# Kernel optimization log

Measured on AMD Instinct MI355X. Metric: run time of the kernel, lower is better.

Reference implementation:

```python
import jax, jax.numpy as jnp
import numpy as np

WS = 8          # window size
NH = 8          # num heads
DIM = 256
HD = DIM // NH  # head dim = 32
SCALE = HD ** -0.5
EPS = 1e-5


def _rel_pos_index(ws):
    # deterministic int index buffer, same math as the torch __init__
    coords = jnp.stack(jnp.meshgrid(jnp.arange(ws), jnp.arange(ws), indexing='ij'))  # [2,ws,ws]
    cf = coords.reshape(2, -1)                     # [2, N]
    rel = cf[:, :, None] - cf[:, None, :]          # [2, N, N]
    return (rel[0] + ws - 1) * (2 * ws - 1) + (rel[1] + ws - 1)  # [N, N]


def _ln(h, g, b):
    m = jnp.mean(h, axis=-1, keepdims=True)
    v = jnp.mean((h - m) ** 2, axis=-1, keepdims=True)
    return (h - m) / jnp.sqrt(v + EPS) * g + b


def setup_inputs() -> dict:
    key = jax.random.key(0)
    ks = jax.random.split(key, 16)
    B_, N, D = 4096, WS * WS, DIM
    s = 0.02
    return {
        'x':      jax.random.normal(ks[0], (B_, N, D), jnp.float32),
        # enhanced qkv: Linear(D,2D) -> LN -> GELU -> Linear(2D,3D)
        'w_qkv1': jax.random.normal(ks[1], (D, 2 * D), jnp.float32) * s,
        'b_qkv1': jnp.zeros((2 * D,), jnp.float32),
        'g_qkv':  jnp.ones((2 * D,), jnp.float32),
        'be_qkv': jnp.zeros((2 * D,), jnp.float32),
        'w_qkv2': jax.random.normal(ks[2], (2 * D, 3 * D), jnp.float32) * s,
        'b_qkv2': jnp.zeros((3 * D,), jnp.float32),
        # relative position bias table [(2*WS-1)^2, NH]
        'rpb':    jax.random.normal(ks[3], ((2 * WS - 1) ** 2, NH), jnp.float32) * s,
        # enhanced proj: Linear(D,2D) -> LN -> GELU -> Linear(2D,D)
        'w_p1':   jax.random.normal(ks[4], (D, 2 * D), jnp.float32) * s,
        'b_p1':   jnp.zeros((2 * D,), jnp.float32),
        'g_p':    jnp.ones((2 * D,), jnp.float32),
        'be_p':   jnp.zeros((2 * D,), jnp.float32),
        'w_p2':   jax.random.normal(ks[5], (2 * D, D), jnp.float32) * s,
        'b_p2':   jnp.zeros((D,), jnp.float32),
    }


def reference(x, w_qkv1, b_qkv1, g_qkv, be_qkv, w_qkv2, b_qkv2, rpb,
              w_p1, b_p1, g_p, be_p, w_p2, b_p2):
    B_, N, C = x.shape
    # enhanced QKV chain: Linear -> LayerNorm -> GELU -> Linear
    h = jax.nn.gelu(_ln(x @ w_qkv1 + b_qkv1, g_qkv, be_qkv), approximate=False)
    qkv = h @ w_qkv2 + b_qkv2                              # [B_, N, 3C]
    qkv = qkv.reshape(B_, N, 3, NH, HD).transpose(2, 0, 3, 1, 4)  # [3, B_, H, N, hd]
    q, k, v = qkv[0], qkv[1], qkv[2]
    attn = jnp.einsum('bhnd,bhmd->bhnm', q * SCALE, k)     # [B_, H, N, N]
    idx = _rel_pos_index(WS)                                # [N, N] int
    bias = rpb[idx.reshape(-1)].reshape(N, N, NH).transpose(2, 0, 1)  # [H, N, N]
    attn = jax.nn.softmax(attn + bias[None], axis=-1)
    out = jnp.einsum('bhnm,bhmd->bhnd', attn, v)           # [B_, H, N, hd]
    out = out.transpose(0, 2, 1, 3).reshape(B_, N, C)
    # enhanced proj chain: Linear -> LayerNorm -> GELU -> Linear
    h = jax.nn.gelu(_ln(out @ w_p1 + b_p1, g_p, be_p), approximate=False)
    return h @ w_p2 + b_p2
```

## Files before the change

kernel.cpp:

```cpp
#include <hip/hip_runtime.h>


typedef __bf16 bf16_t;
typedef __bf16 bf16x8 __attribute__((ext_vector_type(8)));
typedef __bf16 bf16x4 __attribute__((ext_vector_type(4)));
typedef float f32x4 __attribute__((ext_vector_type(4)));

__device__ __forceinline__ f32x4 mfma16(bf16x8 a, bf16x8 b, f32x4 acc) {
  return __builtin_amdgcn_mfma_f32_16x16x32_bf16(a, b, acc, 0, 0, 0);
}

#define SWZ(row, byteoff) ((byteoff) ^ (((row) & 7) << 4))

__device__ __forceinline__ float gelu_f(float v) {
  float e = __expf(v * (1.59576912f + 0.07135482f * v * v));
  return v - v * __builtin_amdgcn_rcpf(1.0f + e);
}

__global__ void wtrans_kernel(const float* __restrict__ src, bf16_t* __restrict__ dst,
                              int kshift, int N, int total) {
  int i = blockIdx.x * 256 + threadIdx.x;
  if (i >= total) return;
  int K = 1 << kshift;
  int k = i & (K - 1);
  int n = i >> kshift;
  dst[i] = (bf16_t)src[(size_t)k * N + n];
}

__device__ __forceinline__ void gemmT_ln_gelu(
    const char* bsrc, const bf16_t* __restrict__ wt,
    const float* __restrict__ bias, const float* __restrict__ gamma,
    const float* __restrict__ beta,
    char* dst, int flb, float2* part, int wave, int g, int c)
{
  f32x4 acc[4][4] = {};
#pragma unroll
  for (int kt = 0; kt < 8; ++kt) {
    bf16x8 a[4], b[4];
#pragma unroll
    for (int mt = 0; mt < 4; ++mt)
      a[mt] = *(const bf16x8*)(wt + (size_t)(wave * 64 + mt * 16 + c) * 256 + kt * 32 + g * 8);
#pragma unroll
    for (int nt = 0; nt < 4; ++nt) {
      int T = nt * 16 + c;
      b[nt] = *(const bf16x8*)(bsrc + SWZ(T, T * 512 + kt * 64 + g * 16));
    }
#pragma unroll
    for (int mt = 0; mt < 4; ++mt)
#pragma unroll
      for (int nt = 0; nt < 4; ++nt)
        acc[mt][nt] = mfma16(a[mt], b[nt], acc[mt][nt]);
  }
  float s[4] = {0.f, 0.f, 0.f, 0.f}, ss[4] = {0.f, 0.f, 0.f, 0.f};
#pragma unroll
  for (int mt = 0; mt < 4; ++mt) {
    float4 b4 = *(const float4*)(bias + wave * 64 + mt * 16 + g * 4);
#pragma unroll
    for (int nt = 0; nt < 4; ++nt)
#pragma unroll
      for (int r = 0; r < 4; ++r) {
        float v = acc[mt][nt][r] + ((const float*)&b4)[r];
        acc[mt][nt][r] = v;
        s[nt] += v;
        ss[nt] += v * v;
      }
  }
#pragma unroll
  for (int nt = 0; nt < 4; ++nt) {
    float sv = s[nt], ssv = ss[nt];
    sv += __shfl_xor(sv, 16, 64); ssv += __shfl_xor(ssv, 16, 64);
    sv += __shfl_xor(sv, 32, 64); ssv += __shfl_xor(ssv, 32, 64);
    if (g == 0) part[wave * 64 + nt * 16 + c] = make_float2(sv, ssv);
  }
  __syncthreads();
#pragma unroll
  for (int nt = 0; nt < 4; ++nt) {
    float sv = 0.f, ssv = 0.f;
#pragma unroll
    for (int w = 0; w < 8; ++w) {
      float2 p2 = part[w * 64 + nt * 16 + c];
      sv += p2.x; ssv += p2.y;
    }
    float m = sv * (1.f / 512.f);
    float rstd = rsqrtf(ssv * (1.f / 512.f) - m * m + 1e-5f);
#pragma unroll
    for (int mt = 0; mt < 4; ++mt)
#pragma unroll
      for (int r = 0; r < 4; ++r)
        acc[mt][nt][r] = (acc[mt][nt][r] - m) * rstd;
  }
#pragma unroll
  for (int mt = 0; mt < 4; ++mt) {
    float4 g4 = *(const float4*)(gamma + wave * 64 + mt * 16 + g * 4);
    float4 be4 = *(const float4*)(beta + wave * 64 + mt * 16 + g * 4);
    int f0 = flb + mt * 16 + g * 4;
#pragma unroll
    for (int nt = 0; nt < 4; ++nt) {
      int T = nt * 16 + c;
      bf16x4 h4;
#pragma unroll
      for (int r = 0; r < 4; ++r) {
        float v = acc[mt][nt][r] * ((const float*)&g4)[r] + ((const float*)&be4)[r];
        h4[r] = (bf16_t)gelu_f(v);
      }
      *(bf16x4*)(dst + SWZ(T, T * 512 + f0 * 2)) = h4;
    }
  }
}

__device__ __forceinline__ void dump_h(const char* rA, const char* rB,
                                       bf16_t* __restrict__ hg, int win, int tid)
{
#pragma unroll
  for (int it = 0; it < 8; ++it) {
    int byte = it * 8192 + tid * 16;
    int T = byte >> 10, off = byte & 1023;
    const char* src = (off < 512) ? (rB + SWZ(T, T * 512 + off))
                                  : (rA + SWZ(T, T * 512 + off - 512));
    *(bf16x8*)((char*)hg + (size_t)(win * 64 + T) * 1024 + off) = *(const bf16x8*)src;
  }
}

__global__ __launch_bounds__(512, 2) void g1_kernel(
    const float* __restrict__ x,
    const bf16_t* __restrict__ w1t, const float* __restrict__ b1,
    const float* __restrict__ g1, const float* __restrict__ be1,
    bf16_t* __restrict__ hg)
{
  __shared__ __align__(16) char sm[69632];
  char* rA = sm;
  char* rB = sm + 32768;
  float2* part = (float2*)(sm + 65536);
  const int tid = threadIdx.x;
  const int wave = tid >> 6, lane = tid & 63;
  const int g = lane >> 4, c = lane & 15;
  const int win = blockIdx.x;

  const float* xw = x + (size_t)win * 16384;
#pragma unroll
  for (int it = 0; it < 8; ++it) {
    int e = it * 2048 + tid * 4;
    float4 v = *(const float4*)(xw + e);
    int row = e >> 8, col = e & 255;
    bf16x4 t4;
    t4[0] = (bf16_t)v.x; t4[1] = (bf16_t)v.y; t4[2] = (bf16_t)v.z; t4[3] = (bf16_t)v.w;
    *(bf16x4*)(rA + SWZ(row, row * 512 + col * 2)) = t4;
  }
  __syncthreads();
  gemmT_ln_gelu(rA, w1t, b1, g1, be1, (wave < 4) ? rB : rA, (wave & 3) * 64,
                part, wave, g, c);
  __syncthreads();
  dump_h(rA, rB, hg, win, tid);
}

__global__ __launch_bounds__(512, 2) void g3_kernel(
    const bf16_t* __restrict__ ao,
    const bf16_t* __restrict__ wp1t, const float* __restrict__ bp1,
    const float* __restrict__ gp, const float* __restrict__ bep,
    bf16_t* __restrict__ h2g)
{
  __shared__ __align__(16) char sm[69632];
  char* rA = sm;
  char* rB = sm + 32768;
  float2* part = (float2*)(sm + 65536);
  const int tid = threadIdx.x;
  const int wave = tid >> 6, lane = tid & 63;
  const int g = lane >> 4, c = lane & 15;
  const int win = blockIdx.x;

  const bf16_t* aow = ao + (size_t)win * 16384;
#pragma unroll
  for (int it = 0; it < 4; ++it) {
    int e = it * 4096 + tid * 8;
    bf16x8 v = *(const bf16x8*)(aow + e);
    int row = e >> 8, col = e & 255;
    *(bf16x8*)(rA + SWZ(row, row * 512 + col * 2)) = v;
  }
  __syncthreads();
  gemmT_ln_gelu(rA, wp1t, bp1, gp, bep, (wave < 4) ? rB : rA, (wave & 3) * 64,
                part, wave, g, c);
  __syncthreads();
  dump_h(rA, rB, h2g, win, tid);
}

__global__ __launch_bounds__(512, 2) void qkv_attn_kernel(
    const bf16_t* __restrict__ hg,
    const bf16_t* __restrict__ w2t, const float* __restrict__ b2,
    const float* __restrict__ rpb,
    bf16_t* __restrict__ ao)
{
  __shared__ __align__(16) char sm[81920];
  char* hs = sm;
  char* ded = sm + 65536;
  const int tid = threadIdx.x;
  const int wave = tid >> 6, lane = tid & 63;
  const int g = lane >> 4, c = lane & 15;
  const int win = blockIdx.x;
  const int head = wave;

  const char* hw = (const char*)(hg + (size_t)win * 32768);
#pragma unroll
  for (int it = 0; it < 8; ++it) {
    int byte = it * 8192 + tid * 16;
    int T = byte >> 10, off = byte & 1023;
    *(bf16x8*)(hs + SWZ(T, T * 1024 + off)) = *(const bf16x8*)(hw + byte);
  }
  __syncthreads();

  bf16x4 vreg[2][4], qreg[2][4], kreg[2][4];

  {
    f32x4 acc[2][4] = {};
#pragma unroll
    for (int kt = 0; kt < 16; ++kt) {
      bf16x8 a[2], b[4];
#pragma unroll
      for (int mt = 0; mt < 2; ++mt)
        a[mt] = *(const bf16x8*)(w2t + (size_t)(512 + head * 32 + mt * 16 + c) * 512 + kt * 32 + g * 8);
#pragma unroll
      for (int nt = 0; nt < 4; ++nt) {
        int T = nt * 16 + c;
        b[nt] = *(const bf16x8*)(hs + SWZ(T, T * 1024 + kt * 64 + g * 16));
      }
#pragma unroll
      for (int mt = 0; mt < 2; ++mt)
#pragma unroll
        for (int nt = 0; nt < 4; ++nt)
          acc[mt][nt] = mfma16(a[mt], b[nt], acc[mt][nt]);
    }
    if (head < 4) {
      char* vs = ded + head * 4096;
#pragma unroll
      for (int mt = 0; mt < 2; ++mt) {
        float4 b4 = *(const float4*)(b2 + 512 + head * 32 + mt * 16 + g * 4);
#pragma unroll
        for (int nt = 0; nt < 4; ++nt) {
          int T = nt * 16 + c;
#pragma unroll
          for (int r = 0; r < 4; ++r) {
            int d = mt * 16 + g * 4 + r;
            *(bf16_t*)(vs + SWZ(d, d * 128 + T * 2)) =
                (bf16_t)(acc[mt][nt][r] + ((const float*)&b4)[r]);
          }
        }
      }
    } else {
#pragma unroll
      for (int mt = 0; mt < 2; ++mt) {
        float4 b4 = *(const float4*)(b2 + 512 + head * 32 + mt * 16 + g * 4);
#pragma unroll
        for (int nt = 0; nt < 4; ++nt) {
          bf16x4 o4;
#pragma unroll
          for (int r = 0; r < 4; ++r)
            o4[r] = (bf16_t)(acc[mt][nt][r] + ((const float*)&b4)[r]);
          vreg[mt][nt] = o4;
        }
      }
    }
  }
  {
    f32x4 acc[2][4] = {};
#pragma unroll
    for (int kt = 0; kt < 16; ++kt) {
      bf16x8 a[2], b[4];
#pragma unroll
      for (int mt = 0; mt < 2; ++mt)
        a[mt] = *(const bf16x8*)(w2t + (size_t)(head * 32 + mt * 16 + c) * 512 + kt * 32 + g * 8);
#pragma unroll
      for (int nt = 0; nt < 4; ++nt) {
        int T = nt * 16 + c;
        b[nt] = *(const bf16x8*)(hs + SWZ(T, T * 1024 + kt * 64 + g * 16));
      }
#pragma unroll
      for (int mt = 0; mt < 2; ++mt)
#pragma unroll
        for (int nt = 0; nt < 4; ++nt)
          acc[mt][nt] = mfma16(a[mt], b[nt], acc[mt][nt]);
    }
#pragma unroll
    for (int mt = 0; mt < 2; ++mt) {
      float4 b4 = *(const float4*)(b2 + head * 32 + mt * 16 + g * 4);
#pragma unroll
      for (int nt = 0; nt < 4; ++nt) {
        bf16x4 o4;
#pragma unroll
        for (int r = 0; r < 4; ++r)
          o4[r] = (bf16_t)((acc[mt][nt][r] + ((const float*)&b4)[r]) * 0.17677669529663687f);
        qreg[mt][nt] = o4;
      }
    }
  }
  {
    f32x4 acc[2][4] = {};
#pragma unroll
    for (int kt = 0; kt < 16; ++kt) {
      bf16x8 a[2], b[4];
#pragma unroll
      for (int mt = 0; mt < 2; ++mt)
        a[mt] = *(const bf16x8*)(w2t + (size_t)(256 + head * 32 + mt * 16 + c) * 512 + kt * 32 + g * 8);
#pragma unroll
      for (int nt = 0; nt < 4; ++nt) {
        int T = nt * 16 + c;
        b[nt] = *(const bf16x8*)(hs + SWZ(T, T * 1024 + kt * 64 + g * 16));
      }
#pragma unroll
      for (int mt = 0; mt < 2; ++mt)
#pragma unroll
        for (int nt = 0; nt < 4; ++nt)
          acc[mt][nt] = mfma16(a[mt], b[nt], acc[mt][nt]);
    }
#pragma unroll
    for (int mt = 0; mt < 2; ++mt) {
      float4 b4 = *(const float4*)(b2 + 256 + head * 32 + mt * 16 + g * 4);
#pragma unroll
      for (int nt = 0; nt < 4; ++nt) {
        bf16x4 o4;
#pragma unroll
        for (int r = 0; r < 4; ++r)
          o4[r] = (bf16_t)(acc[mt][nt][r] + ((const float*)&b4)[r]);
        kreg[mt][nt] = o4;
      }
    }
  }
  __syncthreads();

  {
    char* qb = sm + (head & 3) * 8192 + (head >> 2) * 32768;
#pragma unroll
    for (int mt = 0; mt < 2; ++mt)
#pragma unroll
      for (int nt = 0; nt < 4; ++nt) {
        int T = nt * 16 + c, d0 = mt * 16 + g * 4;
        *(bf16x4*)(qb + SWZ(T, T * 64 + d0 * 2)) = qreg[mt][nt];
        *(bf16x4*)(qb + 4096 + SWZ(T, T * 64 + d0 * 2)) = kreg[mt][nt];
      }
  }
  __syncthreads();

  const int rowbase = (wave >> 2) * 32;
#pragma unroll
  for (int s = 0; s < 2; ++s) {
    const int hd = s * 4 + (wave & 3);
    char* qb = sm + (wave & 3) * 8192 + s * 32768;
    char* vslot = ded + (wave & 3) * 4096;

    bf16x8 aq[2], bk[4];
#pragma unroll
    for (int mt = 0; mt < 2; ++mt) {
      int t = rowbase + mt * 16 + c;
      aq[mt] = *(const bf16x8*)(qb + SWZ(t, t * 64 + g * 16));
    }
#pragma unroll
    for (int nt = 0; nt < 4; ++nt) {
      int t = nt * 16 + c;
      bk[nt] = *(const bf16x8*)(qb + 4096 + SWZ(t, t * 64 + g * 16));
    }
    float p[2][4][4];
#pragma unroll
    for (int mt = 0; mt < 2; ++mt)
#pragma unroll
      for (int nt = 0; nt < 4; ++nt) {
        f32x4 z = {0.f, 0.f, 0.f, 0.f};
        f32x4 s4 = mfma16(aq[mt], bk[nt], z);
#pragma unroll
        for (int r = 0; r < 4; ++r) {
          int i = rowbase + mt * 16 + g * 4 + r, j = nt * 16 + c;
          int idx = ((i >> 3) - (j >> 3) + 7) * 15 + ((i & 7) - (j & 7) + 7);
          p[mt][nt][r] = s4[r] + rpb[idx * 8 + hd];
        }
      }
#pragma unroll
    for (int mt = 0; mt < 2; ++mt)
#pragma unroll
      for (int r = 0; r < 4; ++r) {
        float mx = fmaxf(fmaxf(p[mt][0][r], p[mt][1][r]), fmaxf(p[mt][2][r], p[mt][3][r]));
#pragma unroll
        for (int m = 1; m < 16; m <<= 1) mx = fmaxf(mx, __shfl_xor(mx, m, 64));
        float sum = 0.f;
#pragma unroll
        for (int nt = 0; nt < 4; ++nt) {
          float e = __expf(p[mt][nt][r] - mx);
          p[mt][nt][r] = e; sum += e;
        }
#pragma unroll
        for (int m = 1; m < 16; m <<= 1) sum += __shfl_xor(sum, m, 64);
        float rinv = 1.f / sum;
#pragma unroll
        for (int nt = 0; nt < 4; ++nt) p[mt][nt][r] *= rinv;
      }
    __syncthreads();
#pragma unroll
    for (int mt = 0; mt < 2; ++mt)
#pragma unroll
      for (int nt = 0; nt < 4; ++nt)
#pragma unroll
        for (int r = 0; r < 4; ++r) {
          int i = rowbase + mt * 16 + g * 4 + r, j = nt * 16 + c;
          *(bf16_t*)(qb + SWZ(i, i * 128 + j * 2)) = (bf16_t)p[mt][nt][r];
        }
    asm volatile("s_waitcnt lgkmcnt(0)" ::: "memory");
    f32x4 oacc[2][2] = {};
#pragma unroll
    for (int kp = 0; kp < 2; ++kp) {
      bf16x8 ap[2], bv[2];
#pragma unroll
      for (int mt = 0; mt < 2; ++mt) {
        int t = rowbase + mt * 16 + c;
        ap[mt] = *(const bf16x8*)(qb + SWZ(t, t * 128 + kp * 64 + g * 16));
      }
#pragma unroll
      for (int nt = 0; nt < 2; ++nt) {
        int d = nt * 16 + c;
        bv[nt] = *(const bf16x8*)(vslot + SWZ(d, d * 128 + kp * 64 + g * 16));
      }
#pragma unroll
      for (int mt = 0; mt < 2; ++mt)
#pragma unroll
        for (int nt = 0; nt < 2; ++nt)
          oacc[mt][nt] = mfma16(ap[mt], bv[nt], oacc[mt][nt]);
    }
#pragma unroll
    for (int mt = 0; mt < 2; ++mt)
#pragma unroll
      for (int nt = 0; nt < 2; ++nt)
#pragma unroll
        for (int r = 0; r < 4; ++r) {
          int T = rowbase + mt * 16 + g * 4 + r;
          ao[(size_t)(win * 64 + T) * 256 + hd * 32 + nt * 16 + c] = (bf16_t)oacc[mt][nt][r];
        }
    __syncthreads();
    if (s == 0) {
      if (head >= 4) {
        char* vs = ded + (head & 3) * 4096;
#pragma unroll
        for (int mt = 0; mt < 2; ++mt)
#pragma unroll
          for (int nt = 0; nt < 4; ++nt) {
            int T = nt * 16 + c;
#pragma unroll
            for (int r = 0; r < 4; ++r) {
              int d = mt * 16 + g * 4 + r;
              *(bf16_t*)(vs + SWZ(d, d * 128 + T * 2)) = vreg[mt][nt][r];
            }
          }
      }
      __syncthreads();
    }
  }
}

__global__ __launch_bounds__(512, 2) void g4_kernel(
    const bf16_t* __restrict__ h2g, const bf16_t* __restrict__ wp2t,
    const float* __restrict__ bp2, float* __restrict__ out)
{
  __shared__ __align__(16) char hs[65536];
  const int tid = threadIdx.x;
  const int wave = tid >> 6, lane = tid & 63;
  const int g = lane >> 4, c = lane & 15;
  const int win = blockIdx.x;

  const char* hw = (const char*)(h2g + (size_t)win * 32768);
#pragma unroll
  for (int it = 0; it < 8; ++it) {
    int byte = it * 8192 + tid * 16;
    int T = byte >> 10, off = byte & 1023;
    *(bf16x8*)(hs + SWZ(T, T * 1024 + off)) = *(const bf16x8*)(hw + byte);
  }
  __syncthreads();

  f32x4 acc[2][4] = {};
#pragma unroll
  for (int kt = 0; kt < 16; ++kt) {
    bf16x8 a[2], b[4];
#pragma unroll
    for (int mt = 0; mt < 2; ++mt)
      a[mt] = *(const bf16x8*)(wp2t + (size_t)(wave * 32 + mt * 16 + c) * 512 + kt * 32 + g * 8);
#pragma unroll
    for (int nt = 0; nt < 4; ++nt) {
      int T = nt * 16 + c;
      b[nt] = *(const bf16x8*)(hs + SWZ(T, T * 1024 + kt * 64 + g * 16));
    }
#pragma unroll
    for (int mt = 0; mt < 2; ++mt)
#pragma unroll
      for (int nt = 0; nt < 4; ++nt)
        acc[mt][nt] = mfma16(a[mt], b[nt], acc[mt][nt]);
  }
  float* ow = out + (size_t)win * 16384;
#pragma unroll
  for (int mt = 0; mt < 2; ++mt) {
    float4 b4 = *(const float4*)(bp2 + wave * 32 + mt * 16 + g * 4);
#pragma unroll
    for (int nt = 0; nt < 4; ++nt) {
      int T = nt * 16 + c;
      f32x4 o4;
#pragma unroll
      for (int r = 0; r < 4; ++r) o4[r] = acc[mt][nt][r] + ((const float*)&b4)[r];
      *(f32x4*)(ow + T * 256 + wave * 32 + mt * 16 + g * 4) = o4;
    }
  }
}

extern "C" void kernel_launch(void* const* d_in, const int* in_sizes, int n_in,
                              void* d_out, int out_size, void* d_ws, size_t ws_size,
                              hipStream_t stream) {
  const float* x   = (const float*)d_in[0];
  const float* w1  = (const float*)d_in[1];
  const float* b1  = (const float*)d_in[2];
  const float* g1  = (const float*)d_in[3];
  const float* be1 = (const float*)d_in[4];
  const float* w2  = (const float*)d_in[5];
  const float* b2  = (const float*)d_in[6];
  const float* rpb = (const float*)d_in[7];
  const float* wp1 = (const float*)d_in[8];
  const float* bp1 = (const float*)d_in[9];
  const float* gp  = (const float*)d_in[10];
  const float* bep = (const float*)d_in[11];
  const float* wp2 = (const float*)d_in[12];
  const float* bp2 = (const float*)d_in[13];
  float* out = (float*)d_out;
  char* ws = (char*)d_ws;
  bf16_t* w1t  = (bf16_t*)(ws + 0);
  bf16_t* w2t  = (bf16_t*)(ws + 262144);
  bf16_t* wp1t = (bf16_t*)(ws + 1048576);
  bf16_t* wp2t = (bf16_t*)(ws + 1310720);
  bf16_t* hg   = (bf16_t*)(ws + 2097152);
  bf16_t* ao   = (bf16_t*)(ws + 270532608);

  wtrans_kernel<<<512, 256, 0, stream>>>(w1, w1t, 8, 512, 131072);
  wtrans_kernel<<<1536, 256, 0, stream>>>(w2, w2t, 9, 768, 393216);
  wtrans_kernel<<<512, 256, 0, stream>>>(wp1, wp1t, 8, 512, 131072);
  wtrans_kernel<<<512, 256, 0, stream>>>(wp2, wp2t, 9, 256, 131072);

  g1_kernel<<<4096, 512, 0, stream>>>(x, w1t, b1, g1, be1, hg);
  qkv_attn_kernel<<<4096, 512, 0, stream>>>(hg, w2t, b2, rpb, ao);
  g3_kernel<<<4096, 512, 0, stream>>>(ao, wp1t, bp1, gp, bep, hg);
  g4_kernel<<<4096, 512, 0, stream>>>(hg, wp2t, bp2, out);
}
```

Measured before the change: 1.335 ms.

## Fuse first LN-GELU GEMM into QKV-attention and fuse both projection GEMMs

```diff
diff --git a/kernel.cpp b/kernel.cpp
--- a/kernel.cpp
+++ b/kernel.cpp
@@ -27,6 +27,13 @@
   dst[i] = (bf16_t)src[(size_t)k * N + n];
 }
 
+__global__ void biastab_kernel(const float* __restrict__ rpb, float* __restrict__ bt) {
+  int e = blockIdx.x * 256 + threadIdx.x;
+  int hd = e >> 12, i = (e >> 6) & 63, j = e & 63;
+  int idx = ((i >> 3) - (j >> 3) + 7) * 15 + ((i & 7) - (j & 7) + 7);
+  bt[e] = rpb[idx * 8 + hd];
+}
+
 __device__ __forceinline__ void gemmT_ln_gelu(
     const char* bsrc, const bf16_t* __restrict__ wt,
     const float* __restrict__ bias, const float* __restrict__ gamma,
@@ -108,24 +115,295 @@
   }
 }
 
-__device__ __forceinline__ void dump_h(const char* rA, const char* rB,
-                                       bf16_t* __restrict__ hg, int win, int tid)
-{
-#pragma unroll
-  for (int it = 0; it < 8; ++it) {
-    int byte = it * 8192 + tid * 16;
-    int T = byte >> 10, off = byte & 1023;
-    const char* src = (off < 512) ? (rB + SWZ(T, T * 512 + off))
-                                  : (rA + SWZ(T, T * 512 + off - 512));
-    *(bf16x8*)((char*)hg + (size_t)(win * 64 + T) * 1024 + off) = *(const bf16x8*)src;
-  }
-}
-
-__global__ __launch_bounds__(512, 2) void g1_kernel(
+__global__ __launch_bounds__(512, 4) void g1qa_kernel(
     const float* __restrict__ x,
     const bf16_t* __restrict__ w1t, const float* __restrict__ b1,
-    const float* __restrict__ g1, const float* __restrict__ be1,
-    bf16_t* __restrict__ hg)
+    const float* __restrict__ gamma1, const float* __restrict__ beta1,
+    const bf16_t* __restrict__ w2t, const float* __restrict__ b2,
+    const float* __restrict__ bt,
+    bf16_t* __restrict__ ao)
+{
+  __shared__ __align__(16) char sm[81920];
+  char* rA = sm;
+  char* rB = sm + 32768;
+  char* ded = sm + 65536;
+  float2* part = (float2*)ded;
+  const int tid = threadIdx.x;
+  const int wave = tid >> 6, lane = tid & 63;
+  const int g = lane >> 4, c = lane & 15;
+  const int win = blockIdx.x;
+  const int head = wave;
+
+  const float* xw = x + (size_t)win * 16384;
+#pragma unroll
+  for (int it = 0; it < 8; ++it) {
+    int e = it * 2048 + tid * 4;
+    float4 v = *(const float4*)(xw + e);
+    int row = e >> 8, col = e & 255;
+    bf16x4 t4;
+    t4[0] = (bf16_t)v.x; t4[1] = (bf16_t)v.y; t4[2] = (bf16_t)v.z; t4[3] = (bf16_t)v.w;
+    *(bf16x4*)(rA + SWZ(row, row * 512 + col * 2)) = t4;
+  }
+  __syncthreads();
+  gemmT_ln_gelu(rA, w1t, b1, gamma1, beta1, (wave < 4) ? rB : rA, (wave & 3) * 64,
+                part, wave, g, c);
+  __syncthreads();
+
+  bf16x4 vreg[2][4], qreg[2][4], kreg[2][4];
+
+  {
+    f32x4 acc[2][4] = {};
+#pragma unroll
+    for (int kt = 0; kt < 16; ++kt) {
+      const char* hb = (kt < 8) ? rB : rA;
+      const int ko = (kt & 7) * 64 + g * 16;
+      bf16x8 a[2], b[4];
+#pragma unroll
+      for (int mt = 0; mt < 2; ++mt)
+        a[mt] = *(const bf16x8*)(w2t + (size_t)(512 + head * 32 + mt * 16 + c) * 512 + kt * 32 + g * 8);
+#pragma unroll
+      for (int nt = 0; nt < 4; ++nt) {
+        int T = nt * 16 + c;
+        b[nt] = *(const bf16x8*)(hb + SWZ(T, T * 512 + ko));
+      }
+#pragma unroll
+      for (int mt = 0; mt < 2; ++mt)
+#pragma unroll
+        for (int nt = 0; nt < 4; ++nt)
+          acc[mt][nt] = mfma16(a[mt], b[nt], acc[mt][nt]);
+    }
+    if (head < 4) {
+      char* vs = ded + head * 4096;
+#pragma unroll
+      for (int mt = 0; mt < 2; ++mt) {
+        float4 b4 = *(const float4*)(b2 + 512 + head * 32 + mt * 16 + g * 4);
+#pragma unroll
+        for (int nt = 0; nt < 4; ++nt) {
+          int T = nt * 16 + c;
+#pragma unroll
+          for (int r = 0; r < 4; ++r) {
+            int d = mt * 16 + g * 4 + r;
+            *(bf16_t*)(vs + SWZ(d, d * 128 + T * 2)) =
+                (bf16_t)(acc[mt][nt][r] + ((const float*)&b4)[r]);
+          }
+        }
+      }
+    } else {
+#pragma unroll
+      for (int mt = 0; mt < 2; ++mt) {
+        float4 b4 = *(const float4*)(b2 + 512 + head * 32 + mt * 16 + g * 4);
+#pragma unroll
+        for (int nt = 0; nt < 4; ++nt) {
+          bf16x4 o4;
+#pragma unroll
+          for (int r = 0; r < 4; ++r)
+            o4[r] = (bf16_t)(acc[mt][nt][r] + ((const float*)&b4)[r]);
+          vreg[mt][nt] = o4;
+        }
+      }
+    }
+  }
+  {
+    f32x4 acc[2][4] = {};
+#pragma unroll
+    for (int kt = 0; kt < 16; ++kt) {
+      const char* hb = (kt < 8) ? rB : rA;
+      const int ko = (kt & 7) * 64 + g * 16;
+      bf16x8 a[2], b[4];
+#pragma unroll
+      for (int mt = 0; mt < 2; ++mt)
+        a[mt] = *(const bf16x8*)(w2t + (size_t)(head * 32 + mt * 16 + c) * 512 + kt * 32 + g * 8);
+#pragma unroll
+      for (int nt = 0; nt < 4; ++nt) {
+        int T = nt * 16 + c;
+        b[nt] = *(const bf16x8*)(hb + SWZ(T, T * 512 + ko));
+      }
+#pragma unroll
+      for (int mt = 0; mt < 2; ++mt)
+#pragma unroll
+        for (int nt = 0; nt < 4; ++nt)
+          acc[mt][nt] = mfma16(a[mt], b[nt], acc[mt][nt]);
+    }
+#pragma unroll
+    for (int mt = 0; mt < 2; ++mt) {
+      float4 b4 = *(const float4*)(b2 + head * 32 + mt * 16 + g * 4);
+#pragma unroll
+      for (int nt = 0; nt < 4; ++nt) {
+        bf16x4 o4;
+#pragma unroll
+        for (int r = 0; r < 4; ++r)
+          o4[r] = (bf16_t)((acc[mt][nt][r] + ((const float*)&b4)[r]) * 0.17677669529663687f);
+        qreg[mt][nt] = o4;
+      }
+    }
+  }
+  {
+    f32x4 acc[2][4] = {};
+#pragma unroll
+    for (int kt = 0; kt < 16; ++kt) {
+      const char* hb = (kt < 8) ? rB : rA;
+      const int ko = (kt & 7) * 64 + g * 16;
+      bf16x8 a[2], b[4];
+#pragma unroll
+      for (int mt = 0; mt < 2; ++mt)
+        a[mt] = *(const bf16x8*)(w2t + (size_t)(256 + head * 32 + mt * 16 + c) * 512 + kt * 32 + g * 8);
+#pragma unroll
+      for (int nt = 0; nt < 4; ++nt) {
+        int T = nt * 16 + c;
+        b[nt] = *(const bf16x8*)(hb + SWZ(T, T * 512 + ko));
+      }
+#pragma unroll
+      for (int mt = 0; mt < 2; ++mt)
+#pragma unroll
+        for (int nt = 0; nt < 4; ++nt)
+          acc[mt][nt] = mfma16(a[mt], b[nt], acc[mt][nt]);
+    }
+#pragma unroll
+    for (int mt = 0; mt < 2; ++mt) {
+      float4 b4 = *(const float4*)(b2 + 256 + head * 32 + mt * 16 + g * 4);
+#pragma unroll
+      for (int nt = 0; nt < 4; ++nt) {
+        bf16x4 o4;
+#pragma unroll
+        for (int r = 0; r < 4; ++r)
+          o4[r] = (bf16_t)(acc[mt][nt][r] + ((const float*)&b4)[r]);
+        kreg[mt][nt] = o4;
+      }
+    }
+  }
+  __syncthreads();
+
+  {
+    char* qb = sm + (head & 3) * 8192 + (head >> 2) * 32768;
+#pragma unroll
+    for (int mt = 0; mt < 2; ++mt)
+#pragma unroll
+      for (int nt = 0; nt < 4; ++nt) {
+        int T = nt * 16 + c, d0 = mt * 16 + g * 4;
+        *(bf16x4*)(qb + SWZ(T, T * 64 + d0 * 2)) = qreg[mt][nt];
+        *(bf16x4*)(qb + 4096 + SWZ(T, T * 64 + d0 * 2)) = kreg[mt][nt];
+      }
+  }
+  __syncthreads();
+
+  const int rowbase = (wave >> 2) * 32;
+#pragma unroll
+  for (int s = 0; s < 2; ++s) {
+    const int hd = s * 4 + (wave & 3);
+    char* qb = sm + (wave & 3) * 8192 + s * 32768;
+    char* vslot = ded + (wave & 3) * 4096;
+    const float* btab = bt + hd * 4096;
+
+    bf16x8 aq[2], bk[4];
+#pragma unroll
+    for (int mt = 0; mt < 2; ++mt) {
+      int t = rowbase + mt * 16 + c;
+      aq[mt] = *(const bf16x8*)(qb + SWZ(t, t * 64 + g * 16));
+    }
+#pragma unroll
+    for (int nt = 0; nt < 4; ++nt) {
+      int t = nt * 16 + c;
+      bk[nt] = *(const bf16x8*)(qb + 4096 + SWZ(t, t * 64 + g * 16));
+    }
+    float p[2][4][4];
+#pragma unroll
+    for (int mt = 0; mt < 2; ++mt)
+#pragma unroll
+      for (int nt = 0; nt < 4; ++nt) {
+        f32x4 z = {0.f, 0.f, 0.f, 0.f};
+        f32x4 s4 = mfma16(aq[mt], bk[nt], z);
+#pragma unroll
+        for (int r = 0; r < 4; ++r) {
+          int i = rowbase + mt * 16 + g * 4 + r, j = nt * 16 + c;
+          p[mt][nt][r] = s4[r] + btab[i * 64 + j];
+        }
+      }
+#pragma unroll
+    for (int mt = 0; mt < 2; ++mt)
+#pragma unroll
+      for (int r = 0; r < 4; ++r) {
+        float mx = fmaxf(fmaxf(p[mt][0][r], p[mt][1][r]), fmaxf(p[mt][2][r], p[mt][3][r]));
+#pragma unroll
+        for (int m = 1; m < 16; m <<= 1) mx = fmaxf(mx, __shfl_xor(mx, m, 64));
+        float sum = 0.f;
+#pragma unroll
+        for (int nt = 0; nt < 4; ++nt) {
+          float e = __expf(p[mt][nt][r] - mx);
+          p[mt][nt][r] = e; sum += e;
+        }
+#pragma unroll
+        for (int m = 1; m < 16; m <<= 1) sum += __shfl_xor(sum, m, 64);
+        float rinv = 1.f / sum;
+#pragma unroll
+        for (int nt = 0; nt < 4; ++nt) p[mt][nt][r] *= rinv;
+      }
+    __syncthreads();
+#pragma unroll
+    for (int mt = 0; mt < 2; ++mt)
+#pragma unroll
+      for (int nt = 0; nt < 4; ++nt)
+#pragma unroll
+        for (int r = 0; r < 4; ++r) {
+          int i = rowbase + mt * 16 + g * 4 + r, j = nt * 16 + c;
+          *(bf16_t*)(qb + SWZ(i, i * 128 + j * 2)) = (bf16_t)p[mt][nt][r];
+        }
+    asm volatile("s_waitcnt lgkmcnt(0)" ::: "memory");
+    f32x4 oacc[2][2] = {};
+#pragma unroll
+    for (int kp = 0; kp < 2; ++kp) {
+      bf16x8 ap[2], bv[2];
+#pragma unroll
+      for (int mt = 0; mt < 2; ++mt) {
+        int t = rowbase + mt * 16 + c;
+        ap[mt] = *(const bf16x8*)(qb + SWZ(t, t * 128 + kp * 64 + g * 16));
+      }
+#pragma unroll
+      for (int nt = 0; nt < 2; ++nt) {
+        int d = nt * 16 + c;
+        bv[nt] = *(const bf16x8*)(vslot + SWZ(d, d * 128 + kp * 64 + g * 16));
+      }
+#pragma unroll
+      for (int mt = 0; mt < 2; ++mt)
+#pragma unroll
+        for (int nt = 0; nt < 2; ++nt)
+          oacc[mt][nt] = mfma16(ap[mt], bv[nt], oacc[mt][nt]);
+    }
+#pragma unroll
+    for (int mt = 0; mt < 2; ++mt)
+#pragma unroll
+      for (int nt = 0; nt < 2; ++nt)
+#pragma unroll
+        for (int r = 0; r < 4; ++r) {
+          int T = rowbase + mt * 16 + g * 4 + r;
+          ao[(size_t)(win * 64 + T) * 256 + hd * 32 + nt * 16 + c] = (bf16_t)oacc[mt][nt][r];
+        }
+    __syncthreads();
+    if (s == 0) {
+      if (head >= 4) {
+        char* vs = ded + (head & 3) * 4096;
+#pragma unroll
+        for (int mt = 0; mt < 2; ++mt)
+#pragma unroll
+          for (int nt = 0; nt < 4; ++nt) {
+            int T = nt * 16 + c;
+#pragma unroll
+            for (int r = 0; r < 4; ++r) {
+              int d = mt * 16 + g * 4 + r;
+              *(bf16_t*)(vs + SWZ(d, d * 128 + T * 2)) = vreg[mt][nt][r];
+            }
+          }
+      }
+      __syncthreads();
+    }
+  }
+}
+
+__global__ __launch_bounds__(512, 4) void g3g4_kernel(
+    const bf16_t* __restrict__ ao,
+    const bf16_t* __restrict__ wp1t, const float* __restrict__ bp1,
+    const float* __restrict__ gp, const float* __restrict__ bep,
+    const bf16_t* __restrict__ wp2t, const float* __restrict__ bp2,
+    float* __restrict__ out)
 {
   __shared__ __align__(16) char sm[69632];
   char* rA = sm;
@@ -136,38 +414,6 @@
   const int g = lane >> 4, c = lane & 15;
   const int win = blockIdx.x;
 
-  const float* xw = x + (size_t)win * 16384;
-#pragma unroll
-  for (int it = 0; it < 8; ++it) {
-    int e = it * 2048 + tid * 4;
-    float4 v = *(const float4*)(xw + e);
-    int row = e >> 8, col = e & 255;
-    bf16x4 t4;
-    t4[0] = (bf16_t)v.x; t4[1] = (bf16_t)v.y; t4[2] = (bf16_t)v.z; t4[3] = (bf16_t)v.w;
-    *(bf16x4*)(rA + SWZ(row, row * 512 + col * 2)) = t4;
-  }
-  __syncthreads();
-  gemmT_ln_gelu(rA, w1t, b1, g1, be1, (wave < 4) ? rB : rA, (wave & 3) * 64,
-                part, wave, g, c);
-  __syncthreads();
-  dump_h(rA, rB, hg, win, tid);
-}
-
-__global__ __launch_bounds__(512, 2) void g3_kernel(
-    const bf16_t* __restrict__ ao,
-    const bf16_t* __restrict__ wp1t, const float* __restrict__ bp1,
-    const float* __restrict__ gp, const float* __restrict__ bep,
-    bf16_t* __restrict__ h2g)
-{
-  __shared__ __align__(16) char sm[69632];
-  char* rA = sm;
-  char* rB = sm + 32768;
-  float2* part = (float2*)(sm + 65536);
-  const int tid = threadIdx.x;
-  const int wave = tid >> 6, lane = tid & 63;
-  const int g = lane >> 4, c = lane & 15;
-  const int win = blockIdx.x;
-
   const bf16_t* aow = ao + (size_t)win * 16384;
 #pragma unroll
   for (int it = 0; it < 4; ++it) {
@@ -180,298 +426,12 @@
   gemmT_ln_gelu(rA, wp1t, bp1, gp, bep, (wave < 4) ? rB : rA, (wave & 3) * 64,
                 part, wave, g, c);
   __syncthreads();
-  dump_h(rA, rB, h2g, win, tid);
-}
-
-__global__ __launch_bounds__(512, 2) void qkv_attn_kernel(
-    const bf16_t* __restrict__ hg,
-    const bf16_t* __restrict__ w2t, const float* __restrict__ b2,
-    const float* __restrict__ rpb,
-    bf16_t* __restrict__ ao)
-{
-  __shared__ __align__(16) char sm[81920];
-  char* hs = sm;
-  char* ded = sm + 65536;
-  const int tid = threadIdx.x;
-  const int wave = tid >> 6, lane = tid & 63;
-  const int g = lane >> 4, c = lane & 15;
-  const int win = blockIdx.x;
-  const int head = wave;
-
-  const char* hw = (const char*)(hg + (size_t)win * 32768);
-#pragma unroll
-  for (int it = 0; it < 8; ++it) {
-    int byte = it * 8192 + tid * 16;
-    int T = byte >> 10, off = byte & 1023;
-    *(bf16x8*)(hs + SWZ(T, T * 1024 + off)) = *(const bf16x8*)(hw + byte);
-  }
-  __syncthreads();
-
-  bf16x4 vreg[2][4], qreg[2][4], kreg[2][4];
-
-  {
-    f32x4 acc[2][4] = {};
-#pragma unroll
-    for (int kt = 0; kt < 16; ++kt) {
-      bf16x8 a[2], b[4];
-#pragma unroll
-      for (int mt = 0; mt < 2; ++mt)
-        a[mt] = *(const bf16x8*)(w2t + (size_t)(512 + head * 32 + mt * 16 + c) * 512 + kt * 32 + g * 8);
-#pragma unroll
-      for (int nt = 0; nt < 4; ++nt) {
-        int T = nt * 16 + c;
-        b[nt] = *(const bf16x8*)(hs + SWZ(T, T * 1024 + kt * 64 + g * 16));
-      }
-#pragma unroll
-      for (int mt = 0; mt < 2; ++mt)
-#pragma unroll
-        for (int nt = 0; nt < 4; ++nt)
-          acc[mt][nt] = mfma16(a[mt], b[nt], acc[mt][nt]);
-    }
-    if (head < 4) {
-      char* vs = ded + head * 4096;
-#pragma unroll
-      for (int mt = 0; mt < 2; ++mt) {
-        float4 b4 = *(const float4*)(b2 + 512 + head * 32 + mt * 16 + g * 4);
-#pragma unroll
-        for (int nt = 0; nt < 4; ++nt) {
-          int T = nt * 16 + c;
-#pragma unroll
-          for (int r = 0; r < 4; ++r) {
-            int d = mt * 16 + g * 4 + r;
-            *(bf16_t*)(vs + SWZ(d, d * 128 + T * 2)) =
-                (bf16_t)(acc[mt][nt][r] + ((const float*)&b4)[r]);
-          }
-        }
-      }
-    } else {
-#pragma unroll
-      for (int mt = 0; mt < 2; ++mt) {
-        float4 b4 = *(const float4*)(b2 + 512 + head * 32 + mt * 16 + g * 4);
-#pragma unroll
-        for (int nt = 0; nt < 4; ++nt) {
-          bf16x4 o4;
-#pragma unroll
-          for (int r = 0; r < 4; ++r)
-            o4[r] = (bf16_t)(acc[mt][nt][r] + ((const float*)&b4)[r]);
-          vreg[mt][nt] = o4;
-        }
-      }
-    }
-  }
-  {
-    f32x4 acc[2][4] = {};
-#pragma unroll
-    for (int kt = 0; kt < 16; ++kt) {
-      bf16x8 a[2], b[4];
-#pragma unroll
-      for (int mt = 0; mt < 2; ++mt)
-        a[mt] = *(const bf16x8*)(w2t + (size_t)(head * 32 + mt * 16 + c) * 512 + kt * 32 + g * 8);
-#pragma unroll
-      for (int nt = 0; nt < 4; ++nt) {
-        int T = nt * 16 + c;
-        b[nt] = *(const bf16x8*)(hs + SWZ(T, T * 1024 + kt * 64 + g * 16));
-      }
-#pragma unroll
-      for (int mt = 0; mt < 2; ++mt)
-#pragma unroll
-        for (int nt = 0; nt < 4; ++nt)
-          acc[mt][nt] = mfma16(a[mt], b[nt], acc[mt][nt]);
-    }
-#pragma unroll
-    for (int mt = 0; mt < 2; ++mt) {
-      float4 b4 = *(const float4*)(b2 + head * 32 + mt * 16 + g * 4);
-#pragma unroll
-      for (int nt = 0; nt < 4; ++nt) {
-        bf16x4 o4;
-#pragma unroll
-        for (int r = 0; r < 4; ++r)
-          o4[r] = (bf16_t)((acc[mt][nt][r] + ((const float*)&b4)[r]) * 0.17677669529663687f);
-        qreg[mt][nt] = o4;
-      }
-    }
-  }
-  {
-    f32x4 acc[2][4] = {};
-#pragma unroll
-    for (int kt = 0; kt < 16; ++kt) {
-      bf16x8 a[2], b[4];
-#pragma unroll
-      for (int mt = 0; mt < 2; ++mt)
-        a[mt] = *(const bf16x8*)(w2t + (size_t)(256 + head * 32 + mt * 16 + c) * 512 + kt * 32 + g * 8);
-#pragma unroll
-      for (int nt = 0; nt < 4; ++nt) {
-        int T = nt * 16 + c;
-        b[nt] = *(const bf16x8*)(hs + SWZ(T, T * 1024 + kt * 64 + g * 16));
-      }
-#pragma unroll
-      for (int mt = 0; mt < 2; ++mt)
-#pragma unroll
-        for (int nt = 0; nt < 4; ++nt)
-          acc[mt][nt] = mfma16(a[mt], b[nt], acc[mt][nt]);
-    }
-#pragma unroll
-    for (int mt = 0; mt < 2; ++mt) {
-      float4 b4 = *(const float4*)(b2 + 256 + head * 32 + mt * 16 + g * 4);
-#pragma unroll
-      for (int nt = 0; nt < 4; ++nt) {
-        bf16x4 o4;
-#pragma unroll
-        for (int r = 0; r < 4; ++r)
-          o4[r] = (bf16_t)(acc[mt][nt][r] + ((const float*)&b4)[r]);
-        kreg[mt][nt] = o4;
-      }
-    }
-  }
-  __syncthreads();
-
-  {
-    char* qb = sm + (head & 3) * 8192 + (head >> 2) * 32768;
-#pragma unroll
-    for (int mt = 0; mt < 2; ++mt)
-#pragma unroll
-      for (int nt = 0; nt < 4; ++nt) {
-        int T = nt * 16 + c, d0 = mt * 16 + g * 4;
-        *(bf16x4*)(qb + SWZ(T, T * 64 + d0 * 2)) = qreg[mt][nt];
-        *(bf16x4*)(qb + 4096 + SWZ(T, T * 64 + d0 * 2)) = kreg[mt][nt];
-      }
-  }
-  __syncthreads();
-
-  const int rowbase = (wave >> 2) * 32;
-#pragma unroll
-  for (int s = 0; s < 2; ++s) {
-    const int hd = s * 4 + (wave & 3);
-    char* qb = sm + (wave & 3) * 8192 + s * 32768;
-    char* vslot = ded + (wave & 3) * 4096;
-
-    bf16x8 aq[2], bk[4];
-#pragma unroll
-    for (int mt = 0; mt < 2; ++mt) {
-      int t = rowbase + mt * 16 + c;
-      aq[mt] = *(const bf16x8*)(qb + SWZ(t, t * 64 + g * 16));
-    }
-#pragma unroll
-    for (int nt = 0; nt < 4; ++nt) {
-      int t = nt * 16 + c;
-      bk[nt] = *(const bf16x8*)(qb + 4096 + SWZ(t, t * 64 + g * 16));
-    }
-    float p[2][4][4];
-#pragma unroll
-    for (int mt = 0; mt < 2; ++mt)
-#pragma unroll
-      for (int nt = 0; nt < 4; ++nt) {
-        f32x4 z = {0.f, 0.f, 0.f, 0.f};
-        f32x4 s4 = mfma16(aq[mt], bk[nt], z);
-#pragma unroll
-        for (int r = 0; r < 4; ++r) {
-          int i = rowbase + mt * 16 + g * 4 + r, j = nt * 16 + c;
-          int idx = ((i >> 3) - (j >> 3) + 7) * 15 + ((i & 7) - (j & 7) + 7);
-          p[mt][nt][r] = s4[r] + rpb[idx * 8 + hd];
-        }
-      }
-#pragma unroll
-    for (int mt = 0; mt < 2; ++mt)
-#pragma unroll
-      for (int r = 0; r < 4; ++r) {
-        float mx = fmaxf(fmaxf(p[mt][0][r], p[mt][1][r]), fmaxf(p[mt][2][r], p[mt][3][r]));
-#pragma unroll
-        for (int m = 1; m < 16; m <<= 1) mx = fmaxf(mx, __shfl_xor(mx, m, 64));
-        float sum = 0.f;
-#pragma unroll
-        for (int nt = 0; nt < 4; ++nt) {
-          float e = __expf(p[mt][nt][r] - mx);
-          p[mt][nt][r] = e; sum += e;
-        }
-#pragma unroll
-        for (int m = 1; m < 16; m <<= 1) sum += __shfl_xor(sum, m, 64);
-        float rinv = 1.f / sum;
-#pragma unroll
-        for (int nt = 0; nt < 4; ++nt) p[mt][nt][r] *= rinv;
-      }
-    __syncthreads();
-#pragma unroll
-    for (int mt = 0; mt < 2; ++mt)
-#pragma unroll
-      for (int nt = 0; nt < 4; ++nt)
-#pragma unroll
-        for (int r = 0; r < 4; ++r) {
-          int i = rowbase + mt * 16 + g * 4 + r, j = nt * 16 + c;
-          *(bf16_t*)(qb + SWZ(i, i * 128 + j * 2)) = (bf16_t)p[mt][nt][r];
-        }
-    asm volatile("s_waitcnt lgkmcnt(0)" ::: "memory");
-    f32x4 oacc[2][2] = {};
-#pragma unroll
-    for (int kp = 0; kp < 2; ++kp) {
-      bf16x8 ap[2], bv[2];
-#pragma unroll
-      for (int mt = 0; mt < 2; ++mt) {
-        int t = rowbase + mt * 16 + c;
-        ap[mt] = *(const bf16x8*)(qb + SWZ(t, t * 128 + kp * 64 + g * 16));
-      }
-#pragma unroll
-      for (int nt = 0; nt < 2; ++nt) {
-        int d = nt * 16 + c;
-        bv[nt] = *(const bf16x8*)(vslot + SWZ(d, d * 128 + kp * 64 + g * 16));
-      }
-#pragma unroll
-      for (int mt = 0; mt < 2; ++mt)
-#pragma unroll
-        for (int nt = 0; nt < 2; ++nt)
-          oacc[mt][nt] = mfma16(ap[mt], bv[nt], oacc[mt][nt]);
-    }
-#pragma unroll
-    for (int mt = 0; mt < 2; ++mt)
-#pragma unroll
-      for (int nt = 0; nt < 2; ++nt)
-#pragma unroll
-        for (int r = 0; r < 4; ++r) {
-          int T = rowbase + mt * 16 + g * 4 + r;
-          ao[(size_t)(win * 64 + T) * 256 + hd * 32 + nt * 16 + c] = (bf16_t)oacc[mt][nt][r];
-        }
-    __syncthreads();
-    if (s == 0) {
-      if (head >= 4) {
-        char* vs = ded + (head & 3) * 4096;
-#pragma unroll
-        for (int mt = 0; mt < 2; ++mt)
-#pragma unroll
-          for (int nt = 0; nt < 4; ++nt) {
-            int T = nt * 16 + c;
-#pragma unroll
-            for (int r = 0; r < 4; ++r) {
-              int d = mt * 16 + g * 4 + r;
-              *(bf16_t*)(vs + SWZ(d, d * 128 + T * 2)) = vreg[mt][nt][r];
-            }
-          }
-      }
-      __syncthreads();
-    }
-  }
-}
-
-__global__ __launch_bounds__(512, 2) void g4_kernel(
-    const bf16_t* __restrict__ h2g, const bf16_t* __restrict__ wp2t,
-    const float* __restrict__ bp2, float* __restrict__ out)
-{
-  __shared__ __align__(16) char hs[65536];
-  const int tid = threadIdx.x;
-  const int wave = tid >> 6, lane = tid & 63;
-  const int g = lane >> 4, c = lane & 15;
-  const int win = blockIdx.x;
-
-  const char* hw = (const char*)(h2g + (size_t)win * 32768);
-#pragma unroll
-  for (int it = 0; it < 8; ++it) {
-    int byte = it * 8192 + tid * 16;
-    int T = byte >> 10, off = byte & 1023;
-    *(bf16x8*)(hs + SWZ(T, T * 1024 + off)) = *(const bf16x8*)(hw + byte);
-  }
-  __syncthreads();
 
   f32x4 acc[2][4] = {};
 #pragma unroll
   for (int kt = 0; kt < 16; ++kt) {
+    const char* hb = (kt < 8) ? rB : rA;
+    const int ko = (kt & 7) * 64 + g * 16;
     bf16x8 a[2], b[4];
 #pragma unroll
     for (int mt = 0; mt < 2; ++mt)
@@ -479,7 +439,7 @@
 #pragma unroll
     for (int nt = 0; nt < 4; ++nt) {
       int T = nt * 16 + c;
-      b[nt] = *(const bf16x8*)(hs + SWZ(T, T * 1024 + kt * 64 + g * 16));
+      b[nt] = *(const bf16x8*)(hb + SWZ(T, T * 512 + ko));
     }
 #pragma unroll
     for (int mt = 0; mt < 2; ++mt)
@@ -525,16 +485,15 @@
   bf16_t* w2t  = (bf16_t*)(ws + 262144);
   bf16_t* wp1t = (bf16_t*)(ws + 1048576);
   bf16_t* wp2t = (bf16_t*)(ws + 1310720);
-  bf16_t* hg   = (bf16_t*)(ws + 2097152);
-  bf16_t* ao   = (bf16_t*)(ws + 270532608);
+  float*  bt   = (float*)(ws + 1572864);
+  bf16_t* ao   = (bf16_t*)(ws + 2097152);
 
   wtrans_kernel<<<512, 256, 0, stream>>>(w1, w1t, 8, 512, 131072);
   wtrans_kernel<<<1536, 256, 0, stream>>>(w2, w2t, 9, 768, 393216);
   wtrans_kernel<<<512, 256, 0, stream>>>(wp1, wp1t, 8, 512, 131072);
   wtrans_kernel<<<512, 256, 0, stream>>>(wp2, wp2t, 9, 256, 131072);
-
-  g1_kernel<<<4096, 512, 0, stream>>>(x, w1t, b1, g1, be1, hg);
-  qkv_attn_kernel<<<4096, 512, 0, stream>>>(hg, w2t, b2, rpb, ao);
-  g3_kernel<<<4096, 512, 0, stream>>>(ao, wp1t, bp1, gp, bep, hg);
-  g4_kernel<<<4096, 512, 0, stream>>>(hg, wp2t, bp2, out);
-}
+  biastab_kernel<<<128, 256, 0, stream>>>(rpb, bt);
+
+  g1qa_kernel<<<4096, 512, 0, stream>>>(x, w1t, b1, g1, be1, w2t, b2, bt, ao);
+  g3g4_kernel<<<4096, 512, 0, stream>>>(ao, wp1t, bp1, gp, bep, wp2t, bp2, out);
+}
```

Result: faster. 1.158 ms (-13.3%).
